# Optimization experiments

Hardware: AMD Instinct MI355X
Metric: run time of the kernel (lower is better)

## Reference

```python
import jax, jax.numpy as jnp
import numpy as np

N_NODES = 100000
N_EDGES = 3200000
EMB = 256
OUT = 256


def setup_inputs() -> dict:
    key = jax.random.key(0)
    k1, k2, k3, k4, k5 = jax.random.split(key, 5)
    embeddings = jax.random.normal(k1, (N_NODES, EMB), dtype=jnp.float32)
    adj_rows = jax.random.randint(k2, (N_EDGES,), 0, N_NODES, dtype=jnp.int32)
    adj_cols = jax.random.randint(k3, (N_EDGES,), 0, N_NODES, dtype=jnp.int32)
    adj_vals = jax.random.uniform(k4, (N_EDGES,), dtype=jnp.float32)
    W = jax.random.normal(k5, (EMB, OUT), dtype=jnp.float32) * 0.02
    return {
        "embeddings": embeddings,
        "adj_rows": adj_rows,
        "adj_cols": adj_cols,
        "adj_vals": adj_vals,
        "W": W,
    }


def reference(embeddings, adj_rows, adj_cols, adj_vals, W):
    # SpMM: agg[i] = sum_{e: rows[e]==i} vals[e] * embeddings[cols[e]]
    messages = adj_vals[:, None] * embeddings[adj_cols]  # [E, EMB]
    agg = jax.ops.segment_sum(messages, adj_rows, num_segments=embeddings.shape[0])  # [N, EMB]
    # Dense projection + ReLU
    out = jax.nn.relu(agg @ W)  # [N, OUT]
    return out
```

## Files before the change

kernel.cpp:

```cpp
#include <hip/hip_runtime.h>
#include <stdint.h>


typedef unsigned short u16;
typedef __attribute__((ext_vector_type(8))) short short8v;
typedef __attribute__((ext_vector_type(4))) float f32x4;

#define RBSH 8
#define RB 256
#define NBMAX 512
#define MS_T 4096
#define MS_PT 16

__device__ __forceinline__ float b2f(u16 u) {
  union { unsigned i; float f; } x; x.i = ((unsigned)u) << 16; return x.f;
}
__device__ __forceinline__ u16 f2b(float f) {
  union { unsigned i; float f; } x; x.f = f;
  unsigned r = x.i + 0x7fffu + ((x.i >> 16) & 1u);
  return (u16)(r >> 16);
}
__device__ __forceinline__ float blo(unsigned u) {
  union { unsigned i; float f; } x; x.i = u << 16; return x.f;
}
__device__ __forceinline__ float bhi(unsigned u) {
  union { unsigned i; float f; } x; x.i = u & 0xFFFF0000u; return x.f;
}

__global__ void detect_k(const unsigned* __restrict__ valsw, int* __restrict__ flag) {
  __shared__ int cnt;
  if (threadIdx.x == 0) cnt = 0;
  __syncthreads();
  int c = 0;
  for (int i = threadIdx.x; i < 4096; i += 256) {
    unsigned w = valsw[i];
    if ((w & 0xFFFFu) >= 0x3F80u) c++;
  }
  atomicAdd(&cnt, c);
  __syncthreads();
  if (threadIdx.x == 0) *flag = (cnt < 1024) ? 1 : 0;
}

__global__ __launch_bounds__(256) void count_k(const int* __restrict__ rows,
                                               int* __restrict__ cnt, int E, int NB) {
  __shared__ int h[NBMAX];
  int tid = threadIdx.x;
  for (int b = tid; b < NB; b += 256) h[b] = 0;
  __syncthreads();
  int base = blockIdx.x * MS_T;
#pragma unroll
  for (int i = 0; i < MS_PT; ++i) {
    int e = base + i * 256 + tid;
    if (e < E) atomicAdd(&h[rows[e] >> RBSH], 1);
  }
  __syncthreads();
  for (int b = tid; b < NB; b += 256) cnt[(size_t)blockIdx.x * NB + b] = h[b];
}

__global__ __launch_bounds__(256) void rowscan_k(int* __restrict__ cnt,
                                                 int* __restrict__ totals,
                                                 int NB, int NBLK) {
  __shared__ int part[256];
  int b = blockIdx.x, tid = threadIdx.x;
  int K = (NBLK + 255) >> 8;
  int lo = tid * K;
  int v[8];
  int s = 0;
#pragma unroll
  for (int u = 0; u < 8; ++u) {
    int i = lo + u;
    v[u] = (u < K && i < NBLK) ? cnt[(size_t)i * NB + b] : 0;
    s += v[u];
  }
  part[tid] = s;
  __syncthreads();
  for (int o = 1; o < 256; o <<= 1) {
    int t = (tid >= o) ? part[tid - o] : 0;
    __syncthreads();
    part[tid] += t;
    __syncthreads();
  }
  int run = part[tid] - s;
#pragma unroll
  for (int u = 0; u < 8; ++u) {
    int i = lo + u;
    if (u < K && i < NBLK) cnt[(size_t)i * NB + b] = run;
    run += v[u];
  }
  if (tid == 255) totals[b] = part[255];
}

__global__ __launch_bounds__(512) void boffscan_k(const int* __restrict__ totals,
                                                  int* __restrict__ boffs, int NB) {
  __shared__ int part[512];
  int tid = threadIdx.x;
  int c = (tid < NB) ? totals[tid] : 0;
  part[tid] = c;
  __syncthreads();
  for (int o = 1; o < 512; o <<= 1) {
    int t = (tid >= o) ? part[tid - o] : 0;
    __syncthreads();
    part[tid] += t;
    __syncthreads();
  }
  if (tid < NB) boffs[tid] = part[tid] - c;
  if (tid == 511) boffs[NB] = part[511];
}

__global__ __launch_bounds__(256) void place_k(const int* __restrict__ flag,
                                               const int* __restrict__ rows,
                                               const int* __restrict__ cols,
                                               const void* __restrict__ valsv,
                                               const int* __restrict__ base,
                                               const int* __restrict__ boffs,
                                               int2* __restrict__ pack, int E, int NB) {
  __shared__ int hist[NBMAX + 1];
  __shared__ int gbase[NBMAX];
  __shared__ int part[256];
  __shared__ int2 buf[MS_T];
  __shared__ u16 brow[MS_T];
  int isbf = *flag;
  int tid = threadIdx.x;
  int tbase = blockIdx.x * MS_T;

  for (int b = tid; b <= NB; b += 256) hist[b] = 0;
  for (int b = tid; b < NB; b += 256)
    gbase[b] = boffs[b] + base[(size_t)blockIdx.x * NB + b];
  __syncthreads();

  int bk[MS_PT], ofs[MS_PT], cl[MS_PT], vb[MS_PT];
#pragma unroll
  for (int i = 0; i < MS_PT; ++i) {
    int e = tbase + i * 256 + tid;
    if (e < E) {
      int r = rows[e];
      bk[i] = r >> RBSH;
      cl[i] = cols[e] | ((r & (RB - 1)) << 17);
      float v;
      if (isbf) v = b2f(((const u16*)valsv)[e]);
      else      v = ((const float*)valsv)[e];
      vb[i] = __float_as_int(v);
      ofs[i] = atomicAdd(&hist[bk[i]], 1);
    } else {
      bk[i] = -1; ofs[i] = 0; cl[i] = 0; vb[i] = 0;
    }
  }
  __syncthreads();

  int K = (NB + 255) >> 8;
  int lo = tid * K, hi = lo + K;
  if (hi > NB) hi = NB;
  if (lo > NB) lo = NB;
  int s = 0;
  for (int b = lo; b < hi; ++b) s += hist[b];
  part[tid] = s;
  __syncthreads();
  for (int o = 1; o < 256; o <<= 1) {
    int v = (tid >= o) ? part[tid - o] : 0;
    __syncthreads();
    part[tid] += v;
    __syncthreads();
  }
  int run = part[tid] - s;
  for (int b = lo; b < hi; ++b) {
    int c = hist[b];
    hist[b] = run;
    run += c;
  }
  if (tid == 255) hist[NB] = part[255];
  __syncthreads();

#pragma unroll
  for (int i = 0; i < MS_PT; ++i) {
    if (bk[i] >= 0) {
      int slot = hist[bk[i]] + ofs[i];
      buf[slot] = make_int2(cl[i], vb[i]);
      brow[slot] = (u16)bk[i];
    }
  }
  __syncthreads();

  int tot = hist[NB];
  for (int i = tid; i < tot; i += 256) {
    int b = brow[i];
    pack[gbase[b] + (i - hist[b])] = buf[i];
  }
}

__global__ __launch_bounds__(256) void ms2_k(const int* __restrict__ boffs,
                                             const int2* __restrict__ pack,
                                             int2* __restrict__ pack2,
                                             int* __restrict__ offs, int N, int NB) {
  __shared__ int bins[RB];
  __shared__ int part[256];
  int b = blockIdx.x;
  int tid = threadIdx.x;
  int beg = boffs[b], end = boffs[b + 1];
  bins[tid] = 0;
  __syncthreads();
  for (int i = beg + tid; i < end; i += 256)
    atomicAdd(&bins[(pack[i].x >> 17) & (RB - 1)], 1);
  __syncthreads();
  int c = bins[tid];
  part[tid] = c;
  __syncthreads();
  for (int o = 1; o < 256; o <<= 1) {
    int v = (tid >= o) ? part[tid - o] : 0;
    __syncthreads();
    part[tid] += v;
    __syncthreads();
  }
  int pfx = part[tid] - c;
  __syncthreads();
  int n = b * RB + tid;
  if (n < N) offs[n] = beg + pfx;
  if (b == NB - 1 && tid == 0) offs[N] = end;
  bins[tid] = pfx;
  __syncthreads();
  for (int i = beg + tid; i < end; i += 256) {
    int2 q = pack[i];
    int r = (q.x >> 17) & (RB - 1);
    int p = atomicAdd(&bins[r], 1);
    pack2[beg + p] = q;
  }
}

__global__ void wtr_k(const int* __restrict__ flag, const void* __restrict__ Wv,
                      u16* __restrict__ Wt) {
  int isbf = *flag;
  int i = blockIdx.x * 256 + threadIdx.x;
  int n = i >> 8, k = i & 255;
  float w;
  if (isbf) w = b2f(((const u16*)Wv)[k * 256 + n]);
  else      w = ((const float*)Wv)[k * 256 + n];
  Wt[n * 256 + k] = f2b(w);
}

__global__ __launch_bounds__(256) void proj_k(const int* __restrict__ flag,
                                              const void* __restrict__ embv,
                                              const u16* __restrict__ Wt,
                                              u16* __restrict__ P, int N) {
  int isbf = *flag;
  int wave = threadIdx.x >> 6, lane = threadIdx.x & 63;
  int lr = lane & 15, lq = lane >> 4;
  int m0 = blockIdx.x * 64;
  int n0 = wave * 64;

  f32x4 acc[4][4];
#pragma unroll
  for (int mi = 0; mi < 4; ++mi)
#pragma unroll
    for (int ni = 0; ni < 4; ++ni) acc[mi][ni] = (f32x4)0.f;

  int arow[4];
#pragma unroll
  for (int mi = 0; mi < 4; ++mi) {
    int r = m0 + mi * 16 + lr;
    arow[mi] = r < N ? r : N - 1;
  }

  for (int ks = 0; ks < 8; ++ks) {
    int kb = ks * 32 + lq * 8;
    short8v a[4], b[4];
#pragma unroll
    for (int mi = 0; mi < 4; ++mi) {
      if (isbf) {
        a[mi] = *(const short8v*)((const u16*)embv + (size_t)arow[mi] * 256 + kb);
      } else {
        const float* p = (const float*)embv + (size_t)arow[mi] * 256 + kb;
        float4 x = *(const float4*)p;
        float4 y = *(const float4*)(p + 4);
        short8v t;
        t[0] = (short)f2b(x.x); t[1] = (short)f2b(x.y);
        t[2] = (short)f2b(x.z); t[3] = (short)f2b(x.w);
        t[4] = (short)f2b(y.x); t[5] = (short)f2b(y.y);
        t[6] = (short)f2b(y.z); t[7] = (short)f2b(y.w);
        a[mi] = t;
      }
    }
#pragma unroll
    for (int ni = 0; ni < 4; ++ni)
      b[ni] = *(const short8v*)(Wt + (size_t)(n0 + ni * 16 + lr) * 256 + kb);
#pragma unroll
    for (int mi = 0; mi < 4; ++mi)
#pragma unroll
      for (int ni = 0; ni < 4; ++ni)
        acc[mi][ni] = __builtin_amdgcn_mfma_f32_16x16x32_bf16(a[mi], b[ni], acc[mi][ni], 0, 0, 0);
  }

#pragma unroll
  for (int mi = 0; mi < 4; ++mi) {
    int rbase = m0 + mi * 16 + lq * 4;
#pragma unroll
    for (int ni = 0; ni < 4; ++ni) {
      int col = n0 + ni * 16 + lr;
#pragma unroll
      for (int r = 0; r < 4; ++r) {
        int row = rbase + r;
        if (row < N) P[(size_t)row * 256 + col] = f2b(acc[mi][ni][r]);
      }
    }
  }
}

__global__ __launch_bounds__(256) void agg_k(const int* __restrict__ flag,
                                             const u16* __restrict__ P,
                                             const int* __restrict__ offs,
                                             const int2* __restrict__ pack,
                                             void* __restrict__ outv, int N) {
  int outbf = *flag;
  int wave = threadIdx.x >> 6, lane = threadIdx.x & 63;
  int node = blockIdx.x * 4 + wave;
  if (node >= N) return;
  int sub = lane & 31, half = lane >> 5;
  int beg = offs[node], end = offs[node + 1];
  const u16* pb = P + sub * 8;

  float acc[8];
#pragma unroll
  for (int k = 0; k < 8; ++k) acc[k] = 0.f;

  for (int j = beg; j < end; j += 16) {
#pragma unroll
    for (int k = 0; k < 8; ++k) {
      int i0 = j + 2 * k + half;
      int ic = i0 < end ? i0 : end - 1;
      int2 q = pack[ic];
      float v = i0 < end ? __int_as_float(q.y) : 0.f;
      const int4* src = (const int4*)(pb + (size_t)(q.x & 0x1FFFF) * 256);
      int4 u = *src;
      acc[0] += v * blo((unsigned)u.x); acc[1] += v * bhi((unsigned)u.x);
      acc[2] += v * blo((unsigned)u.y); acc[3] += v * bhi((unsigned)u.y);
      acc[4] += v * blo((unsigned)u.z); acc[5] += v * bhi((unsigned)u.z);
      acc[6] += v * blo((unsigned)u.w); acc[7] += v * bhi((unsigned)u.w);
    }
  }

#pragma unroll
  for (int k = 0; k < 8; ++k) acc[k] += __shfl(acc[k], lane ^ 32);

#pragma unroll
  for (int k = 0; k < 8; ++k) acc[k] = fmaxf(acc[k], 0.f);
  int d0 = sub * 8 + half * 4;
  if (outbf) {
    ushort4 o;
    o.x = f2b(acc[half * 4 + 0]); o.y = f2b(acc[half * 4 + 1]);
    o.z = f2b(acc[half * 4 + 2]); o.w = f2b(acc[half * 4 + 3]);
    *(ushort4*)((u16*)outv + (size_t)node * 256 + d0) = o;
  } else {
    float4 o;
    o.x = acc[half * 4 + 0]; o.y = acc[half * 4 + 1];
    o.z = acc[half * 4 + 2]; o.w = acc[half * 4 + 3];
    *(float4*)((float*)outv + (size_t)node * 256 + d0) = o;
  }
}


extern "C" void kernel_launch(void* const* d_in, const int* in_sizes, int n_in,
                              void* d_out, int out_size, void* d_ws, size_t ws_size,
                              hipStream_t stream) {
  const void* emb  = d_in[0];
  const int*  rows = (const int*)d_in[1];
  const int*  cols = (const int*)d_in[2];
  const void* vals = d_in[3];
  const void* W    = d_in[4];

  int N = in_sizes[0] / 256;
  int E = in_sizes[1];
  int NB = (N + RB - 1) >> RBSH;
  int NBLK = (E + MS_T - 1) / MS_T;

  char* ws = (char*)d_ws;
  size_t off = 0;
  auto carve = [&](size_t bytes) -> char* {
    char* p = ws + off;
    off += (bytes + 511) & ~(size_t)511;
    return p;
  };
  int*  flag   = (int*) carve(4);
  int*  cnt    = (int*) carve((size_t)NBLK * NB * 4);
  int*  totals = (int*) carve((size_t)NB * 4);
  int*  boffs  = (int*) carve((size_t)(NB + 1) * 4);
  int*  offs   = (int*) carve((size_t)(N + 1) * 4);
  int2* pack   = (int2*)carve((size_t)E * 8);
  int2* pack2  = (int2*)carve((size_t)E * 8);
  u16*  P      = (u16*) carve((size_t)N * 256 * 2);
  u16*  Wt     = (u16*) carve((size_t)256 * 256 * 2);
  (void)ws_size; (void)n_in; (void)out_size;

  detect_k<<<1, 256, 0, stream>>>((const unsigned*)vals, flag);

  count_k<<<NBLK, 256, 0, stream>>>(rows, cnt, E, NB);
  rowscan_k<<<NB, 256, 0, stream>>>(cnt, totals, NB, NBLK);
  boffscan_k<<<1, 512, 0, stream>>>(totals, boffs, NB);

  wtr_k<<<256, 256, 0, stream>>>(flag, W, Wt);

  int pb = (N + 63) / 64;
  proj_k<<<pb, 256, 0, stream>>>(flag, emb, Wt, P, N);

  place_k<<<NBLK, 256, 0, stream>>>(flag, rows, cols, vals, cnt, boffs, pack, E, NB);

  ms2_k<<<NB, 256, 0, stream>>>(boffs, pack, pack2, offs, N, NB);

  int ab = (N + 3) / 4;
  agg_k<<<ab, 256, 0, stream>>>(flag, P, offs, pack2, d_out, N);
}
```

Measured before the change: 586.3 us.

## Batch gather loads in agg_k, fuse detection into count_k, retune sort kernels

The aggregation inner loop now issues all eight edge-record loads first, then all eight embedding-row loads, then the FMAs. Scheduling barriers keep that grouping so more gathers are in flight at once. The separate dtype-detection kernel is folded into block 0 of count_k, removing one launch. The multisplit tile is halved, which doubles the number of count/place blocks, and ms2_k now runs with 512 threads per block. These trade launch and latency overhead for more registers in agg_k and a larger per-block count matrix to scan.

```diff
diff --git a/kernel.cpp b/kernel.cpp
--- a/kernel.cpp
+++ b/kernel.cpp
@@ -9,8 +9,8 @@
 #define RBSH 8
 #define RB 256
 #define NBMAX 512
-#define MS_T 4096
-#define MS_PT 16
+#define MS_T 2048
+#define MS_PT 8
 
 __device__ __forceinline__ float b2f(u16 u) {
   union { unsigned i; float f; } x; x.i = ((unsigned)u) << 16; return x.f;
@@ -27,26 +27,25 @@
   union { unsigned i; float f; } x; x.i = u & 0xFFFF0000u; return x.f;
 }
 
-__global__ void detect_k(const unsigned* __restrict__ valsw, int* __restrict__ flag) {
-  __shared__ int cnt;
-  if (threadIdx.x == 0) cnt = 0;
-  __syncthreads();
-  int c = 0;
-  for (int i = threadIdx.x; i < 4096; i += 256) {
-    unsigned w = valsw[i];
-    if ((w & 0xFFFFu) >= 0x3F80u) c++;
-  }
-  atomicAdd(&cnt, c);
-  __syncthreads();
-  if (threadIdx.x == 0) *flag = (cnt < 1024) ? 1 : 0;
-}
-
 __global__ __launch_bounds__(256) void count_k(const int* __restrict__ rows,
+                                               const unsigned* __restrict__ valsw,
+                                               int* __restrict__ flag,
                                                int* __restrict__ cnt, int E, int NB) {
   __shared__ int h[NBMAX];
+  __shared__ int dcnt;
   int tid = threadIdx.x;
   for (int b = tid; b < NB; b += 256) h[b] = 0;
-  __syncthreads();
+  if (blockIdx.x == 0 && tid == 0) dcnt = 0;
+  __syncthreads();
+  if (blockIdx.x == 0) {
+    int dlim = E < 4096 ? E : 4096;
+    int c = 0;
+    for (int i = tid; i < dlim; i += 256) {
+      unsigned w = valsw[i];
+      if ((w & 0xFFFFu) >= 0x3F80u) c++;
+    }
+    atomicAdd(&dcnt, c);
+  }
   int base = blockIdx.x * MS_T;
 #pragma unroll
   for (int i = 0; i < MS_PT; ++i) {
@@ -55,6 +54,10 @@
   }
   __syncthreads();
   for (int b = tid; b < NB; b += 256) cnt[(size_t)blockIdx.x * NB + b] = h[b];
+  if (blockIdx.x == 0 && tid == 0) {
+    int dlim = E < 4096 ? E : 4096;
+    *flag = (dcnt < (dlim >> 2)) ? 1 : 0;
+  }
 }
 
 __global__ __launch_bounds__(256) void rowscan_k(int* __restrict__ cnt,
@@ -187,7 +190,7 @@
   }
 }
 
-__global__ __launch_bounds__(256) void ms2_k(const int* __restrict__ boffs,
+__global__ __launch_bounds__(512) void ms2_k(const int* __restrict__ boffs,
                                              const int2* __restrict__ pack,
                                              int2* __restrict__ pack2,
                                              int* __restrict__ offs, int N, int NB) {
@@ -196,28 +199,29 @@
   int b = blockIdx.x;
   int tid = threadIdx.x;
   int beg = boffs[b], end = boffs[b + 1];
-  bins[tid] = 0;
-  __syncthreads();
-  for (int i = beg + tid; i < end; i += 256)
+  if (tid < RB) bins[tid] = 0;
+  __syncthreads();
+  for (int i = beg + tid; i < end; i += 512)
     atomicAdd(&bins[(pack[i].x >> 17) & (RB - 1)], 1);
   __syncthreads();
-  int c = bins[tid];
-  part[tid] = c;
+  int c = (tid < 256) ? bins[tid] : 0;
+  if (tid < 256) part[tid] = c;
   __syncthreads();
   for (int o = 1; o < 256; o <<= 1) {
-    int v = (tid >= o) ? part[tid - o] : 0;
-    __syncthreads();
-    part[tid] += v;
-    __syncthreads();
-  }
-  int pfx = part[tid] - c;
-  __syncthreads();
-  int n = b * RB + tid;
-  if (n < N) offs[n] = beg + pfx;
+    int v = (tid < 256 && tid >= o) ? part[tid - o] : 0;
+    __syncthreads();
+    if (tid < 256) part[tid] += v;
+    __syncthreads();
+  }
+  if (tid < 256) {
+    int pfx = part[tid] - c;
+    int n = b * RB + tid;
+    if (n < N) offs[n] = beg + pfx;
+    bins[tid] = pfx;
+  }
   if (b == NB - 1 && tid == 0) offs[N] = end;
-  bins[tid] = pfx;
-  __syncthreads();
-  for (int i = beg + tid; i < end; i += 256) {
+  __syncthreads();
+  for (int i = beg + tid; i < end; i += 512) {
     int2 q = pack[i];
     int r = (q.x >> 17) & (RB - 1);
     int p = atomicAdd(&bins[r], 1);
@@ -321,19 +325,24 @@
   for (int k = 0; k < 8; ++k) acc[k] = 0.f;
 
   for (int j = beg; j < end; j += 16) {
-#pragma unroll
-    for (int k = 0; k < 8; ++k) {
-      int i0 = j + 2 * k + half;
-      int ic = i0 < end ? i0 : end - 1;
-      int2 q = pack[ic];
-      float v = i0 < end ? __int_as_float(q.y) : 0.f;
-      const int4* src = (const int4*)(pb + (size_t)(q.x & 0x1FFFF) * 256);
-      int4 u = *src;
-      acc[0] += v * blo((unsigned)u.x); acc[1] += v * bhi((unsigned)u.x);
-      acc[2] += v * blo((unsigned)u.y); acc[3] += v * bhi((unsigned)u.y);
-      acc[4] += v * blo((unsigned)u.z); acc[5] += v * bhi((unsigned)u.z);
-      acc[6] += v * blo((unsigned)u.w); acc[7] += v * bhi((unsigned)u.w);
-    }
+#define LDQ(k) int i##k = j + 2 * k + half; \
+               int2 q##k = pack[i##k < end ? i##k : end - 1];
+    LDQ(0) LDQ(1) LDQ(2) LDQ(3) LDQ(4) LDQ(5) LDQ(6) LDQ(7)
+#undef LDQ
+    __builtin_amdgcn_sched_barrier(0);
+#define LDU(k) int4 u##k = *(const int4*)(pb + (size_t)(q##k.x & 0x1FFFF) * 256); \
+               float v##k = i##k < end ? __int_as_float(q##k.y) : 0.f;
+    LDU(0) LDU(1) LDU(2) LDU(3) LDU(4) LDU(5) LDU(6) LDU(7)
+#undef LDU
+    __builtin_amdgcn_sched_barrier(0);
+#define FMA8(k) { unsigned ux = (unsigned)u##k.x, uy = (unsigned)u##k.y; \
+                  unsigned uz = (unsigned)u##k.z, uw = (unsigned)u##k.w; \
+                  acc[0] += v##k * blo(ux); acc[1] += v##k * bhi(ux); \
+                  acc[2] += v##k * blo(uy); acc[3] += v##k * bhi(uy); \
+                  acc[4] += v##k * blo(uz); acc[5] += v##k * bhi(uz); \
+                  acc[6] += v##k * blo(uw); acc[7] += v##k * bhi(uw); }
+    FMA8(0) FMA8(1) FMA8(2) FMA8(3) FMA8(4) FMA8(5) FMA8(6) FMA8(7)
+#undef FMA8
   }
 
 #pragma unroll
@@ -388,9 +397,7 @@
   u16*  Wt     = (u16*) carve((size_t)256 * 256 * 2);
   (void)ws_size; (void)n_in; (void)out_size;
 
-  detect_k<<<1, 256, 0, stream>>>((const unsigned*)vals, flag);
-
-  count_k<<<NBLK, 256, 0, stream>>>(rows, cnt, E, NB);
+  count_k<<<NBLK, 256, 0, stream>>>(rows, (const unsigned*)vals, flag, cnt, E, NB);
   rowscan_k<<<NB, 256, 0, stream>>>(cnt, totals, NB, NBLK);
   boffscan_k<<<1, 512, 0, stream>>>(totals, boffs, NB);
 
@@ -401,7 +408,7 @@
 
   place_k<<<NBLK, 256, 0, stream>>>(flag, rows, cols, vals, cnt, boffs, pack, E, NB);
 
-  ms2_k<<<NB, 256, 0, stream>>>(boffs, pack, pack2, offs, N, NB);
+  ms2_k<<<NB, 512, 0, stream>>>(boffs, pack, pack2, offs, N, NB);
 
   int ab = (N + 3) / 4;
   agg_k<<<ab, 256, 0, stream>>>(flag, P, offs, pack2, d_out, N);
```

After: 566.9 us. 3.3% less time.
